# Kernel tuning notes

Measured on AMD Instinct MI355X. Metric: run time of the kernel, lower is better.

## Reference

```python
import jax, jax.numpy as jnp
import numpy as np

VOCAB = 100000
HID = 256
BATCH = 4096
TOTAL_TOKENS = 819200
BN_EPS = 1e-5


def setup_inputs() -> dict:
    key = jax.random.key(0)
    ks = jax.random.split(key, 8)
    token_ids = jax.random.randint(ks[0], (TOTAL_TOKENS,), 0, VOCAB, dtype=jnp.int64)
    segment_ids = jnp.sort(jax.random.randint(ks[1], (TOTAL_TOKENS,), 0, BATCH, dtype=jnp.int64))
    labels = jax.random.uniform(ks[2], (BATCH,), dtype=jnp.float32)
    emb = jax.random.normal(ks[3], (VOCAB, HID), dtype=jnp.float32)
    W1 = jax.random.normal(ks[4], (HID, HID), dtype=jnp.float32) * (1.0 / np.sqrt(HID))
    b1 = jnp.zeros((HID,), dtype=jnp.float32)
    gamma = jnp.ones((HID,), dtype=jnp.float32)
    beta = jnp.zeros((HID,), dtype=jnp.float32)
    W2 = jax.random.normal(ks[5], (1, HID), dtype=jnp.float32) * (1.0 / np.sqrt(HID))
    b2 = jnp.zeros((1,), dtype=jnp.float32)
    return {"token_ids": token_ids, "segment_ids": segment_ids, "labels": labels,
            "emb": emb, "W1": W1, "b1": b1, "gamma": gamma, "beta": beta,
            "W2": W2, "b2": b2}


def reference(token_ids, segment_ids, labels, emb, W1, b1, gamma, beta, W2, b2):
    # Ragged embedding gather + per-document mean (fused EmbeddingBag-mean).
    tok_emb = emb[token_ids]                                   # [T, H]
    seg_sum = jax.ops.segment_sum(tok_emb, segment_ids, num_segments=BATCH)  # [B, H]
    counts = jax.ops.segment_sum(jnp.ones((token_ids.shape[0],), tok_emb.dtype),
                                 segment_ids, num_segments=BATCH)            # [B]
    bow = seg_sum / jnp.maximum(counts, 1.0)[:, None]          # [B, H]
    # Linear -> BatchNorm1d (batch stats, biased var) -> ReLU
    h = bow @ W1.T + b1                                        # [B, H]
    mu = jnp.mean(h, axis=0)
    var = jnp.mean((h - mu) ** 2, axis=0)
    h = (h - mu) * jax.lax.rsqrt(var + BN_EPS) * gamma + beta
    h = jax.nn.relu(h)
    # Dropout in eval mode (identity) for deterministic reference.
    logits = (h @ W2.T + b2)[:, 0]                             # [B]
    # BCEWithLogitsLoss (mean), numerically stable form.
    loss = jnp.mean(jnp.maximum(logits, 0.0) - logits * labels
                    + jnp.log1p(jnp.exp(-jnp.abs(logits))))
    return (loss, logits)
```

## Files before the change

kernel.cpp:

```cpp
#include <hip/hip_runtime.h>
#include <hip/hip_fp16.h>
#include <math.h>

#define VOCAB 100000
#define HID 256
#define BATCH 4096
#define BN_EPS 1e-5f
#define TPB1 512
#define ROWS2 8
#define KT 16

#define WS_SEGSUM 0
#define WS_COUNTS (BATCH * HID)
#define WS_COLSUM (WS_COUNTS + BATCH)
#define WS_COLSQ  (WS_COLSUM + HID)
#define WS_ZERO_FLOATS (WS_COLSQ + HID)
#define WS_EMB16_OFF_BYTES ((size_t)WS_ZERO_FLOATS * 4)
#define WS_FP16_BYTES_NEEDED (WS_EMB16_OFF_BYTES + (size_t)VOCAB * HID * 2)

__global__ __launch_bounds__(256) void k0_convert(
    const float* __restrict__ emb, __half* __restrict__ emb16, int n4)
{
    int i = blockIdx.x * 256 + threadIdx.x;
    if (i >= n4) return;
    float4 v = reinterpret_cast<const float4*>(emb)[i];
    __half2 a = __halves2half2(__float2half_rn(v.x), __float2half_rn(v.y));
    __half2 b = __halves2half2(__float2half_rn(v.z), __float2half_rn(v.w));
    uint2 o;
    o.x = __builtin_bit_cast(unsigned int, a);
    o.y = __builtin_bit_cast(unsigned int, b);
    reinterpret_cast<uint2*>(emb16)[i] = o;
}

__global__ __launch_bounds__(256) void k1_gather_fp16(
    const int* __restrict__ token_ids, const int* __restrict__ segment_ids,
    const __half* __restrict__ emb16, float* __restrict__ seg_sum,
    float* __restrict__ counts, int T)
{
    __shared__ int s_tok[TPB1];
    __shared__ int s_seg[TPB1];
    const int tid = threadIdx.x;
    const int t0  = blockIdx.x * TPB1;
    const int n   = min(TPB1, T - t0);
    if (n <= 0) return;
    for (int i = tid; i < n; i += 256) {
        s_tok[i] = token_ids[t0 + i];
        s_seg[i] = segment_ids[t0 + i];
    }
    __syncthreads();

    const int wave = tid >> 6;
    const int lane = tid & 63;
    const int per  = TPB1 / 4;
    const int start = wave * per;
    const int end   = min(start + per, n);
    if (start >= end) return;

    const uint2* __restrict__ embv = reinterpret_cast<const uint2*>(emb16);
    float4 acc = make_float4(0.f, 0.f, 0.f, 0.f);
    int cur = s_seg[start];
    int runlen = 0;

#define K1_FLUSH() do {                                                        \
        float* p = &seg_sum[(size_t)cur * HID + lane * 4];                     \
        atomicAdd(p + 0, acc.x); atomicAdd(p + 1, acc.y);                      \
        atomicAdd(p + 2, acc.z); atomicAdd(p + 3, acc.w);                      \
        if (lane == 0) atomicAdd(&counts[cur], (float)runlen);                 \
        acc = make_float4(0.f, 0.f, 0.f, 0.f); runlen = 0;                     \
    } while (0)

#define K1_PROC16(ii, u) do {                                                  \
        int seg = s_seg[ii];                  \
        if (seg != cur) { K1_FLUSH(); cur = seg; }                             \
        __half2 h01 = __builtin_bit_cast(__half2, (u).x);                      \
        __half2 h23 = __builtin_bit_cast(__half2, (u).y);                      \
        float2 f01 = __half22float2(h01);                                      \
        float2 f23 = __half22float2(h23);                                      \
        acc.x += f01.x; acc.y += f01.y; acc.z += f23.x; acc.w += f23.y;        \
        runlen++;                                                              \
    } while (0)

    const int m8 = start + ((end - start) & ~7);
    for (int i = start; i < m8; i += 8) {
        uint2 u0 = embv[(size_t)s_tok[i + 0] * 64 + lane];
        uint2 u1 = embv[(size_t)s_tok[i + 1] * 64 + lane];
        uint2 u2 = embv[(size_t)s_tok[i + 2] * 64 + lane];
        uint2 u3 = embv[(size_t)s_tok[i + 3] * 64 + lane];
        uint2 u4 = embv[(size_t)s_tok[i + 4] * 64 + lane];
        uint2 u5 = embv[(size_t)s_tok[i + 5] * 64 + lane];
        uint2 u6 = embv[(size_t)s_tok[i + 6] * 64 + lane];
        uint2 u7 = embv[(size_t)s_tok[i + 7] * 64 + lane];
        K1_PROC16(i + 0, u0); K1_PROC16(i + 1, u1);
        K1_PROC16(i + 2, u2); K1_PROC16(i + 3, u3);
        K1_PROC16(i + 4, u4); K1_PROC16(i + 5, u5);
        K1_PROC16(i + 6, u6); K1_PROC16(i + 7, u7);
    }
    for (int i = m8; i < end; ++i) {
        uint2 u = embv[(size_t)s_tok[i] * 64 + lane];
        K1_PROC16(i, u);
    }
    K1_FLUSH();
#undef K1_PROC16
#undef K1_FLUSH
}

__global__ __launch_bounds__(256) void k1_gather_fp32(
    const int* __restrict__ token_ids, const int* __restrict__ segment_ids,
    const float* __restrict__ emb, float* __restrict__ seg_sum,
    float* __restrict__ counts, int T)
{
    __shared__ int s_tok[TPB1];
    __shared__ int s_seg[TPB1];
    const int tid = threadIdx.x;
    const int t0  = blockIdx.x * TPB1;
    const int n   = min(TPB1, T - t0);
    if (n <= 0) return;
    for (int i = tid; i < n; i += 256) {
        s_tok[i] = token_ids[t0 + i];
        s_seg[i] = segment_ids[t0 + i];
    }
    __syncthreads();

    const int wave = tid >> 6;
    const int lane = tid & 63;
    const int per  = TPB1 / 4;
    const int start = wave * per;
    const int end   = min(start + per, n);
    if (start >= end) return;

    const float4* __restrict__ embv = reinterpret_cast<const float4*>(emb);
    float4 acc = make_float4(0.f, 0.f, 0.f, 0.f);
    int cur = s_seg[start];
    int runlen = 0;

#define K1_FLUSH() do {                                                        \
        float* p = &seg_sum[(size_t)cur * HID + lane * 4];                     \
        atomicAdd(p + 0, acc.x); atomicAdd(p + 1, acc.y);                      \
        atomicAdd(p + 2, acc.z); atomicAdd(p + 3, acc.w);                      \
        if (lane == 0) atomicAdd(&counts[cur], (float)runlen);                 \
        acc = make_float4(0.f, 0.f, 0.f, 0.f); runlen = 0;                     \
    } while (0)

#define K1_PROC(ii, v) do {                                                    \
        int seg = s_seg[ii];                                                   \
        if (seg != cur) { K1_FLUSH(); cur = seg; }                             \
        acc.x += (v).x; acc.y += (v).y; acc.z += (v).z; acc.w += (v).w;        \
        runlen++;                                                              \
    } while (0)

    const int m4 = start + ((end - start) & ~3);
    for (int i = start; i < m4; i += 4) {
        float4 a0 = embv[(size_t)s_tok[i + 0] * 64 + lane];
        float4 a1 = embv[(size_t)s_tok[i + 1] * 64 + lane];
        float4 a2 = embv[(size_t)s_tok[i + 2] * 64 + lane];
        float4 a3 = embv[(size_t)s_tok[i + 3] * 64 + lane];
        K1_PROC(i + 0, a0); K1_PROC(i + 1, a1);
        K1_PROC(i + 2, a2); K1_PROC(i + 3, a3);
    }
    for (int i = m4; i < end; ++i) {
        float4 a = embv[(size_t)s_tok[i] * 64 + lane];
        K1_PROC(i, a);
    }
    K1_FLUSH();
#undef K1_PROC
#undef K1_FLUSH
}

__global__ __launch_bounds__(256) void k2_gemm_bn_partial(
    const float* seg_sum, const float* __restrict__ counts,
    const float* __restrict__ W1, const float* __restrict__ b1,
    float* hout, float* __restrict__ colsum, float* __restrict__ colsq,
    float* __restrict__ out)
{
    __shared__ float s_bow[ROWS2][HID];
    __shared__ float s_w1t[KT][HID + 1];
    const int tid = threadIdx.x;
    const int b0  = blockIdx.x * ROWS2;

    if (blockIdx.x == 0 && tid == 0) out[0] = 0.f;

#pragma unroll
    for (int r = 0; r < ROWS2; ++r) {
        float c   = counts[b0 + r];
        float inv = 1.f / fmaxf(c, 1.f);
        s_bow[r][tid] = seg_sum[(size_t)(b0 + r) * HID + tid] * inv;
    }

    const int jrow = tid >> 2;
    const int kq   = tid & 3;
    const float4* __restrict__ W1v4 = reinterpret_cast<const float4*>(W1);

    float acc[ROWS2];
    const float bj = b1[tid];
#pragma unroll
    for (int r = 0; r < ROWS2; ++r) acc[r] = bj;

    float4 pre[4];
#pragma unroll
    for (int p = 0; p < 4; ++p)
        pre[p] = W1v4[(size_t)(p * 64 + jrow) * 64 + kq];

    for (int kt = 0; kt < HID / KT; ++kt) {
        __syncthreads();
#pragma unroll
        for (int p = 0; p < 4; ++p) {
            int j = p * 64 + jrow;
            s_w1t[kq * 4 + 0][j] = pre[p].x;
            s_w1t[kq * 4 + 1][j] = pre[p].y;
            s_w1t[kq * 4 + 2][j] = pre[p].z;
            s_w1t[kq * 4 + 3][j] = pre[p].w;
        }
        __syncthreads();
        if (kt + 1 < HID / KT) {
#pragma unroll
            for (int p = 0; p < 4; ++p)
                pre[p] = W1v4[(size_t)(p * 64 + jrow) * 64 + (kt + 1) * 4 + kq];
        }
#pragma unroll
        for (int q = 0; q < 4; ++q) {
            float w0 = s_w1t[q * 4 + 0][tid];
            float w1 = s_w1t[q * 4 + 1][tid];
            float w2 = s_w1t[q * 4 + 2][tid];
            float w3 = s_w1t[q * 4 + 3][tid];
#pragma unroll
            for (int r = 0; r < ROWS2; ++r) {
                float4 bb = *reinterpret_cast<const float4*>(
                    &s_bow[r][kt * KT + q * 4]);
                acc[r] = fmaf(bb.x, w0,
                         fmaf(bb.y, w1,
                         fmaf(bb.z, w2,
                         fmaf(bb.w, w3, acc[r]))));
            }
        }
    }

    float ls = 0.f, lq = 0.f;
#pragma unroll
    for (int r = 0; r < ROWS2; ++r) {
        float v = acc[r];
        hout[(size_t)(b0 + r) * HID + tid] = v;
        ls += v;
        lq += v * v;
    }
    atomicAdd(&colsum[tid], ls);
    atomicAdd(&colsq[tid], lq);
}

__global__ __launch_bounds__(256) void k5_bn_relu_logits_loss(
    const float* __restrict__ hmat,
    const float* __restrict__ colsum, const float* __restrict__ colsq,
    const float* __restrict__ gamma, const float* __restrict__ beta,
    const float* __restrict__ W2, const float* __restrict__ b2,
    const float* __restrict__ labels, float* __restrict__ out)
{
    __shared__ float s_loss[4];
    const int tid  = threadIdx.x;
    const int w    = tid >> 6;
    const int lane = tid & 63;
    const int b0   = blockIdx.x * 16 + w * 4;

    const int j0 = lane, j1 = lane + 64, j2 = lane + 128, j3 = lane + 192;

#define BN_SS(jj, sc, sh) \
    { float mu = colsum[jj] * (1.f / BATCH); \
      float vr = colsq[jj] * (1.f / BATCH) - mu * mu; \
      sc = gamma[jj] * rsqrtf(vr + BN_EPS); \
      sh = beta[jj] - mu * sc; }
    float sc0, sh0, sc1, sh1, sc2, sh2, sc3, sh3;
    BN_SS(j0, sc0, sh0); BN_SS(j1, sc1, sh1);
    BN_SS(j2, sc2, sh2); BN_SS(j3, sc3, sh3);
#undef BN_SS

    const float w0 = W2[j0], w1 = W2[j1], w2v = W2[j2], w3 = W2[j3];
    const float bias2 = b2[0];

    float bce_acc = 0.f;
#pragma unroll
    for (int rr = 0; rr < 4; ++rr) {
        const int b = b0 + rr;
        const float* hr = hmat + (size_t)b * HID;
        float h0 = hr[j0], h1 = hr[j1], h2 = hr[j2], h3 = hr[j3];
        float s = 0.f;
        s += fmaxf(fmaf(h0, sc0, sh0), 0.f) * w0;
        s += fmaxf(fmaf(h1, sc1, sh1), 0.f) * w1;
        s += fmaxf(fmaf(h2, sc2, sh2), 0.f) * w2v;
        s += fmaxf(fmaf(h3, sc3, sh3), 0.f) * w3;
#pragma unroll
        for (int off = 32; off > 0; off >>= 1)
            s += __shfl_down(s, off, 64);
        if (lane == 0) {
            float z = s + bias2;
            out[1 + b] = z;
            float lb = labels[b];
            bce_acc += fmaxf(z, 0.f) - z * lb + log1pf(expf(-fabsf(z)));
        }
    }
    if (lane == 0) s_loss[w] = bce_acc;
    __syncthreads();
    if (tid == 0) {
        float t = (s_loss[0] + s_loss[1]) + (s_loss[2] + s_loss[3]);
        atomicAdd(&out[0], t * (1.f / BATCH));
    }
}

extern "C" void kernel_launch(void* const* d_in, const int* in_sizes, int n_in,
                              void* d_out, int out_size, void* d_ws, size_t ws_size,
                              hipStream_t stream)
{
    const int*   token_ids   = (const int*)d_in[0];
    const int*   segment_ids = (const int*)d_in[1];
    const float* labels      = (const float*)d_in[2];
    const float* emb         = (const float*)d_in[3];
    const float* W1          = (const float*)d_in[4];
    const float* b1          = (const float*)d_in[5];
    const float* gamma       = (const float*)d_in[6];
    const float* beta        = (const float*)d_in[7];
    const float* W2          = (const float*)d_in[8];
    const float* b2          = (const float*)d_in[9];
    float* out = (float*)d_out;
    float* ws  = (float*)d_ws;

    float* seg_sum = ws + WS_SEGSUM;
    float* counts  = ws + WS_COUNTS;
    float* colsum  = ws + WS_COLSUM;
    float* colsq   = ws + WS_COLSQ;

    const int T = in_sizes[0];
    const int g1 = (T + TPB1 - 1) / TPB1;

    hipMemsetAsync(d_ws, 0, (size_t)WS_ZERO_FLOATS * sizeof(float), stream);

    if (ws_size >= WS_FP16_BYTES_NEEDED) {
        __half* emb16 = (__half*)((char*)d_ws + WS_EMB16_OFF_BYTES);
        const int n4 = VOCAB * HID / 4;
        k0_convert<<<(n4 + 255) / 256, 256, 0, stream>>>(emb, emb16, n4);
        k1_gather_fp16<<<g1, 256, 0, stream>>>(token_ids, segment_ids, emb16,
                                               seg_sum, counts, T);
    } else {
        k1_gather_fp32<<<g1, 256, 0, stream>>>(token_ids, segment_ids, emb,
                                               seg_sum, counts, T);
    }
    k2_gemm_bn_partial<<<BATCH / ROWS2, 256, 0, stream>>>(
        seg_sum, counts, W1, b1, seg_sum, colsum, colsq, out);
    k5_bn_relu_logits_loss<<<BATCH / 16, 256, 0, stream>>>(
        seg_sum, colsum, colsq, gamma, beta, W2, b2, labels, out);
}
```

Measured before the change: 284.2 us.

## Fold workspace zeroing into convert kernel and register-tile the W1 GEMM

The workspace memset is removed and the zeroing is done inside the fp16 conversion kernel, which saves a separate memset launch. The GEMM kernel now handles 16 rows per block with a 4x4 register tile per thread, using float4 shared-memory reads and a 32-wide K tile. Column sums are reduced in shared memory before the global atomics. These changes cut W1 reloads, shared-memory traffic per FMA and global atomic contention, at the cost of more registers and a larger shared footprint. The GEMM is a small part of the total next to the gather and conversion.

```diff
diff --git a/kernel.cpp b/kernel.cpp
--- a/kernel.cpp
+++ b/kernel.cpp
@@ -7,8 +7,6 @@
 #define BATCH 4096
 #define BN_EPS 1e-5f
 #define TPB1 512
-#define ROWS2 8
-#define KT 16
 
 #define WS_SEGSUM 0
 #define WS_COUNTS (BATCH * HID)
@@ -18,10 +16,12 @@
 #define WS_EMB16_OFF_BYTES ((size_t)WS_ZERO_FLOATS * 4)
 #define WS_FP16_BYTES_NEEDED (WS_EMB16_OFF_BYTES + (size_t)VOCAB * HID * 2)
 
-__global__ __launch_bounds__(256) void k0_convert(
-    const float* __restrict__ emb, __half* __restrict__ emb16, int n4)
+__global__ __launch_bounds__(256) void k0_convert_zero(
+    const float* __restrict__ emb, __half* __restrict__ emb16,
+    float4* __restrict__ zws, int n4, int nz4)
 {
     int i = blockIdx.x * 256 + threadIdx.x;
+    if (i < nz4) zws[i] = make_float4(0.f, 0.f, 0.f, 0.f);
     if (i >= n4) return;
     float4 v = reinterpret_cast<const float4*>(emb)[i];
     __half2 a = __halves2half2(__float2half_rn(v.x), __float2half_rn(v.y));
@@ -166,84 +166,122 @@
 #undef K1_FLUSH
 }
 
-__global__ __launch_bounds__(256) void k2_gemm_bn_partial(
+#define KT2 32
+__global__ __launch_bounds__(256) void k2_gemm_bn(
     const float* seg_sum, const float* __restrict__ counts,
     const float* __restrict__ W1, const float* __restrict__ b1,
     float* hout, float* __restrict__ colsum, float* __restrict__ colsq,
     float* __restrict__ out)
 {
-    __shared__ float s_bow[ROWS2][HID];
-    __shared__ float s_w1t[KT][HID + 1];
+    __shared__ float s_bow[16][HID];
+    __shared__ float s_w1t[KT2][HID + 1];
+    __shared__ float s_cs[HID];
+    __shared__ float s_cq[HID];
     const int tid = threadIdx.x;
-    const int b0  = blockIdx.x * ROWS2;
+    const int b0  = blockIdx.x * 16;
 
     if (blockIdx.x == 0 && tid == 0) out[0] = 0.f;
-
-#pragma unroll
-    for (int r = 0; r < ROWS2; ++r) {
-        float c   = counts[b0 + r];
-        float inv = 1.f / fmaxf(c, 1.f);
-        s_bow[r][tid] = seg_sum[(size_t)(b0 + r) * HID + tid] * inv;
-    }
-
-    const int jrow = tid >> 2;
-    const int kq   = tid & 3;
-    const float4* __restrict__ W1v4 = reinterpret_cast<const float4*>(W1);
-
-    float acc[ROWS2];
-    const float bj = b1[tid];
-#pragma unroll
-    for (int r = 0; r < ROWS2; ++r) acc[r] = bj;
-
-    float4 pre[4];
-#pragma unroll
-    for (int p = 0; p < 4; ++p)
-        pre[p] = W1v4[(size_t)(p * 64 + jrow) * 64 + kq];
-
-    for (int kt = 0; kt < HID / KT; ++kt) {
+    s_cs[tid] = 0.f;
+    s_cq[tid] = 0.f;
+
+    const float4* ss4 = reinterpret_cast<const float4*>(seg_sum + (size_t)b0 * HID);
+#pragma unroll
+    for (int p = 0; p < 4; ++p) {
+        int f  = p * 256 + tid;
+        int r  = f >> 6, k4 = f & 63;
+        float inv = 1.f / fmaxf(counts[b0 + r], 1.f);
+        float4 v = ss4[f];
+        v.x *= inv; v.y *= inv; v.z *= inv; v.w *= inv;
+        *reinterpret_cast<float4*>(&s_bow[r][k4 * 4]) = v;
+    }
+
+    const int jr = tid >> 3;
+    const int q  = tid & 7;
+    const float4* __restrict__ W1v = reinterpret_cast<const float4*>(W1);
+
+    float4 pre[8];
+#pragma unroll
+    for (int pass = 0; pass < 8; ++pass)
+        pre[pass] = W1v[(size_t)(pass * 32 + jr) * 64 + q];
+
+    const int cg = tid & 63;
+    const int rg = tid >> 6;
+
+    float acc[4][4];
+    {
+        float4 bj = reinterpret_cast<const float4*>(b1)[cg];
+#pragma unroll
+        for (int r = 0; r < 4; ++r) {
+            acc[r][0] = bj.x; acc[r][1] = bj.y;
+            acc[r][2] = bj.z; acc[r][3] = bj.w;
+        }
+    }
+
+    for (int kt = 0; kt < HID / KT2; ++kt) {
         __syncthreads();
 #pragma unroll
-        for (int p = 0; p < 4; ++p) {
-            int j = p * 64 + jrow;
-            s_w1t[kq * 4 + 0][j] = pre[p].x;
-            s_w1t[kq * 4 + 1][j] = pre[p].y;
-            s_w1t[kq * 4 + 2][j] = pre[p].z;
-            s_w1t[kq * 4 + 3][j] = pre[p].w;
+        for (int pass = 0; pass < 8; ++pass) {
+            int j = pass * 32 + jr;
+            float4 w = pre[pass];
+            int kl = q * 4;
+            s_w1t[kl + 0][j] = w.x;
+            s_w1t[kl + 1][j] = w.y;
+            s_w1t[kl + 2][j] = w.z;
+            s_w1t[kl + 3][j] = w.w;
         }
         __syncthreads();
-        if (kt + 1 < HID / KT) {
-#pragma unroll
-            for (int p = 0; p < 4; ++p)
-                pre[p] = W1v4[(size_t)(p * 64 + jrow) * 64 + (kt + 1) * 4 + kq];
-        }
-#pragma unroll
-        for (int q = 0; q < 4; ++q) {
-            float w0 = s_w1t[q * 4 + 0][tid];
-            float w1 = s_w1t[q * 4 + 1][tid];
-            float w2 = s_w1t[q * 4 + 2][tid];
-            float w3 = s_w1t[q * 4 + 3][tid];
-#pragma unroll
-            for (int r = 0; r < ROWS2; ++r) {
-                float4 bb = *reinterpret_cast<const float4*>(
-                    &s_bow[r][kt * KT + q * 4]);
-                acc[r] = fmaf(bb.x, w0,
-                         fmaf(bb.y, w1,
-                         fmaf(bb.z, w2,
-                         fmaf(bb.w, w3, acc[r]))));
-            }
-        }
-    }
-
-    float ls = 0.f, lq = 0.f;
-#pragma unroll
-    for (int r = 0; r < ROWS2; ++r) {
-        float v = acc[r];
-        hout[(size_t)(b0 + r) * HID + tid] = v;
-        ls += v;
-        lq += v * v;
-    }
-    atomicAdd(&colsum[tid], ls);
-    atomicAdd(&colsq[tid], lq);
+        if (kt + 1 < HID / KT2) {
+#pragma unroll
+            for (int pass = 0; pass < 8; ++pass)
+                pre[pass] = W1v[(size_t)(pass * 32 + jr) * 64 + (kt + 1) * 8 + q];
+        }
+#pragma unroll
+        for (int ks = 0; ks < 8; ++ks) {
+            const int kg = kt * KT2 + ks * 4;
+            const int kl = ks * 4;
+            float4 bb0 = *reinterpret_cast<const float4*>(&s_bow[rg * 4 + 0][kg]);
+            float4 bb1 = *reinterpret_cast<const float4*>(&s_bow[rg * 4 + 1][kg]);
+            float4 bb2 = *reinterpret_cast<const float4*>(&s_bow[rg * 4 + 2][kg]);
+            float4 bb3 = *reinterpret_cast<const float4*>(&s_bow[rg * 4 + 3][kg]);
+            float4 w0 = *reinterpret_cast<const float4*>(&s_w1t[kl + 0][cg * 4]);
+            float4 w1 = *reinterpret_cast<const float4*>(&s_w1t[kl + 1][cg * 4]);
+            float4 w2 = *reinterpret_cast<const float4*>(&s_w1t[kl + 2][cg * 4]);
+            float4 w3 = *reinterpret_cast<const float4*>(&s_w1t[kl + 3][cg * 4]);
+#define K2_ROW(r, bb)                                                          \
+            acc[r][0] = fmaf(bb.x, w0.x, fmaf(bb.y, w1.x,                      \
+                        fmaf(bb.z, w2.x, fmaf(bb.w, w3.x, acc[r][0]))));       \
+            acc[r][1] = fmaf(bb.x, w0.y, fmaf(bb.y, w1.y,                      \
+                        fmaf(bb.z, w2.y, fmaf(bb.w, w3.y, acc[r][1]))));       \
+            acc[r][2] = fmaf(bb.x, w0.z, fmaf(bb.y, w1.z,                      \
+                        fmaf(bb.z, w2.z, fmaf(bb.w, w3.z, acc[r][2]))));       \
+            acc[r][3] = fmaf(bb.x, w0.w, fmaf(bb.y, w1.w,                      \
+                        fmaf(bb.z, w2.w, fmaf(bb.w, w3.w, acc[r][3]))));
+            K2_ROW(0, bb0)
+            K2_ROW(1, bb1)
+            K2_ROW(2, bb2)
+            K2_ROW(3, bb3)
+#undef K2_ROW
+        }
+    }
+
+#pragma unroll
+    for (int r = 0; r < 4; ++r) {
+        float4 v;
+        v.x = acc[r][0]; v.y = acc[r][1]; v.z = acc[r][2]; v.w = acc[r][3];
+        *reinterpret_cast<float4*>(
+            &hout[(size_t)(b0 + rg * 4 + r) * HID + cg * 4]) = v;
+    }
+#pragma unroll
+    for (int c = 0; c < 4; ++c) {
+        float ps  = ((acc[0][c] + acc[1][c]) + (acc[2][c] + acc[3][c]));
+        float psq = ((acc[0][c] * acc[0][c] + acc[1][c] * acc[1][c])
+                   + (acc[2][c] * acc[2][c] + acc[3][c] * acc[3][c]));
+        atomicAdd(&s_cs[cg * 4 + c], ps);
+        atomicAdd(&s_cq[cg * 4 + c], psq);
+    }
+    __syncthreads();
+    atomicAdd(&colsum[tid], s_cs[tid]);
+    atomicAdd(&colsq[tid], s_cq[tid]);
 }
 
 __global__ __launch_bounds__(256) void k5_bn_relu_logits_loss(
@@ -328,19 +366,20 @@
     const int T = in_sizes[0];
     const int g1 = (T + TPB1 - 1) / TPB1;
 
-    hipMemsetAsync(d_ws, 0, (size_t)WS_ZERO_FLOATS * sizeof(float), stream);
-
     if (ws_size >= WS_FP16_BYTES_NEEDED) {
         __half* emb16 = (__half*)((char*)d_ws + WS_EMB16_OFF_BYTES);
-        const int n4 = VOCAB * HID / 4;
-        k0_convert<<<(n4 + 255) / 256, 256, 0, stream>>>(emb, emb16, n4);
+        const int n4  = VOCAB * HID / 4;
+        const int nz4 = WS_ZERO_FLOATS / 4;
+        k0_convert_zero<<<(n4 + 255) / 256, 256, 0, stream>>>(
+            emb, emb16, (float4*)d_ws, n4, nz4);
         k1_gather_fp16<<<g1, 256, 0, stream>>>(token_ids, segment_ids, emb16,
                                                seg_sum, counts, T);
     } else {
+        hipMemsetAsync(d_ws, 0, (size_t)WS_ZERO_FLOATS * sizeof(float), stream);
         k1_gather_fp32<<<g1, 256, 0, stream>>>(token_ids, segment_ids, emb,
                                                seg_sum, counts, T);
     }
-    k2_gemm_bn_partial<<<BATCH / ROWS2, 256, 0, stream>>>(
+    k2_gemm_bn<<<BATCH / 16, 256, 0, stream>>>(
         seg_sum, counts, W1, b1, seg_sum, colsum, colsq, out);
     k5_bn_relu_logits_loss<<<BATCH / 16, 256, 0, stream>>>(
         seg_sum, colsum, colsq, gamma, beta, W2, b2, labels, out);
```

Result: no change. 279.5 us (median of 2 runs) (-1.7%).
